# Optimization experiments

Hardware: AMD Instinct MI355X
Metric: run time of the kernel (lower is better)

The kernel has to match this reference:

```python
import jax, jax.numpy as jnp
import numpy as np

N_NODES = 100000


def gcn_conv(x, src, dst, W, b):
    # x: [N, F_in]; src/dst include self-loops; symmetric degree normalization (PyG GCNConv)
    n = x.shape[0]
    xw = x @ W  # [N, F_out]
    ones = jnp.ones(dst.shape[0], dtype=xw.dtype)
    deg = jax.ops.segment_sum(ones, dst, num_segments=n)  # in-degree incl. self-loop
    dinv = jnp.where(deg > 0, jax.lax.rsqrt(deg), 0.0)
    norm = dinv[src] * dinv[dst]  # [E]
    msg = xw[src] * norm[:, None]  # gather + per-edge scale
    out = jax.ops.segment_sum(msg, dst, num_segments=n)  # scatter-add aggregation
    return out + b


def setup_inputs() -> dict:
    key = jax.random.key(0)
    ks = jax.random.split(key, 6)
    F_in = 512
    E = 3200000
    x = jax.random.normal(ks[0], (N_NODES, F_in), dtype=jnp.float32)
    edge_index = jax.random.randint(ks[1], (2, E), 0, N_NODES, dtype=jnp.int64)
    W1 = jax.random.normal(ks[2], (F_in, 16), dtype=jnp.float32) * (1.0 / np.sqrt(F_in))
    b1 = jnp.zeros((16,), dtype=jnp.float32)
    W2 = jax.random.normal(ks[3], (16, 16), dtype=jnp.float32) * 0.25
    b2 = jnp.zeros((16,), dtype=jnp.float32)
    fc_w = jax.random.normal(ks[4], (16, 1), dtype=jnp.float32) * 0.25
    fc_b = jnp.zeros((1,), dtype=jnp.float32)
    return {"x": x, "edge_index": edge_index, "W1": W1, "b1": b1,
            "W2": W2, "b2": b2, "fc_w": fc_w, "fc_b": fc_b}


def reference(x, edge_index, W1, b1, W2, b2, fc_w, fc_b):
    n = x.shape[0]
    loop = jnp.arange(n, dtype=edge_index.dtype)
    src = jnp.concatenate([edge_index[0], loop])  # add self-loops
    dst = jnp.concatenate([edge_index[1], loop])
    h = jax.nn.relu(gcn_conv(x, src, dst, W1, b1))
    h = jax.nn.relu(gcn_conv(h, src, dst, W2, b2))
    g = jnp.mean(h, axis=0, keepdims=True)  # global_mean_pool, single graph -> [1, 16]
    return g @ fc_w + fc_b  # [1, 1]
```

## Files before the change

kernel.cpp:

```cpp
#include <hip/hip_runtime.h>
#include <hip/hip_fp16.h>
#include <stdint.h>

#define F_IN 512
#define F_OUT 16
#define CB_SHIFT 8
#define CB_W 256
#define PER 6250
#define SORT_CAP 6400

__device__ inline float4 f4_shfl_xor(float4 v, int mask) {
    float4 r;
    r.x = __shfl_xor(v.x, mask);
    r.y = __shfl_xor(v.y, mask);
    r.z = __shfl_xor(v.z, mask);
    r.w = __shfl_xor(v.w, mask);
    return r;
}

__device__ inline float4 ld_h4(const __half* __restrict__ xw, int s, int q) {
    const __half2* p = (const __half2*)(xw + ((size_t)s << 4)) + (q << 1);
    float2 f0 = __half22float2(p[0]);
    float2 f1 = __half22float2(p[1]);
    return make_float4(f0.x, f0.y, f1.x, f1.y);
}

__global__ __launch_bounds__(256) void k_chist(const int* __restrict__ ei, int E, int K1, int B,
                                               int* __restrict__ cntT) {
    __shared__ int h[512];
    int t = threadIdx.x;
    for (int i = t; i < K1; i += 256) h[i] = 0;
    __syncthreads();
    int e0 = blockIdx.x * PER, e1 = min(E, e0 + PER);
    for (int e = e0 + t; e < e1; e += 256)
        atomicAdd(&h[ei[(size_t)E + e] >> CB_SHIFT], 1);
    __syncthreads();
    for (int i = t; i < K1; i += 256) cntT[(size_t)i * B + blockIdx.x] = h[i];
}

__global__ __launch_bounds__(512) void k_btot(const int* __restrict__ cntT, int B, int K1,
                                              int* __restrict__ bucketBase, int* __restrict__ bucketCnt) {
    __shared__ int sm[512];
    int k = threadIdx.x;
    int tot = 0;
    if (k < K1) {
        const int4* row = (const int4*)(cntT + (size_t)k * B);
        for (int b = 0; b < B / 4; b++) {
            int4 v = row[b];
            tot += v.x + v.y + v.z + v.w;
        }
    }
    sm[k] = tot;
    __syncthreads();
    for (int off = 1; off < 512; off <<= 1) {
        int add = (k >= off) ? sm[k - off] : 0;
        __syncthreads();
        sm[k] += add;
        __syncthreads();
    }
    if (k < K1) { bucketBase[k] = sm[k] - tot; bucketCnt[k] = tot; }
}

__global__ __launch_bounds__(512) void k_bbase(const int* __restrict__ cntT, int B,
                                               const int* __restrict__ bucketBase,
                                               int* __restrict__ baseT) {
    __shared__ int sm[512];
    int k = blockIdx.x, t = threadIdx.x;
    int v = (t < B) ? cntT[(size_t)k * B + t] : 0;
    sm[t] = v;
    __syncthreads();
    for (int off = 1; off < 512; off <<= 1) {
        int add = (t >= off) ? sm[t - off] : 0;
        __syncthreads();
        sm[t] += add;
        __syncthreads();
    }
    if (t < B) baseT[(size_t)k * B + t] = bucketBase[k] + sm[t] - v;
}

__global__ __launch_bounds__(512) void k_csort(const int* __restrict__ ei, int E, int K1, int B,
                                               const int* __restrict__ baseT, unsigned* __restrict__ part) {
    __shared__ unsigned sorted[SORT_CAP];
    __shared__ int h[512], lb[512], cur[512], gb[512];
    int t = threadIdx.x;
    int e0 = blockIdx.x * PER, e1 = min(E, e0 + PER);
    h[t] = 0;
    __syncthreads();
    for (int e = e0 + t; e < e1; e += 512)
        atomicAdd(&h[ei[(size_t)E + e] >> CB_SHIFT], 1);
    __syncthreads();
    int v = h[t];
    lb[t] = v;
    __syncthreads();
    for (int off = 1; off < 512; off <<= 1) {
        int add = (t >= off) ? lb[t - off] : 0;
        __syncthreads();
        lb[t] += add;
        __syncthreads();
    }
    int excl = lb[t] - v;
    __syncthreads();
    lb[t] = excl;
    cur[t] = excl;
    if (t < K1) gb[t] = baseT[(size_t)t * B + blockIdx.x];
    __syncthreads();
    for (int e = e0 + t; e < e1; e += 512) {
        int s = ei[e];
        int d = ei[(size_t)E + e];
        int pos = atomicAdd(&cur[d >> CB_SHIFT], 1);
        sorted[pos] = ((unsigned)s << CB_SHIFT) | (unsigned)(d & (CB_W - 1));
    }
    __syncthreads();
    int g16 = t >> 4, ln = t & 15;
    for (int k = g16; k < K1; k += 32) {
        int s0 = lb[k];
        int s1 = cur[k];
        int g  = gb[k];
        for (int i = s0 + ln; i < s1; i += 16)
            part[(size_t)g + (i - s0)] = sorted[i];
    }
}

__global__ __launch_bounds__(512) void k_prep2(const unsigned* __restrict__ part,
                                               const int* __restrict__ bucketBase, const int* __restrict__ bucketCnt,
                                               int* __restrict__ hist, float* __restrict__ dinv,
                                               int* __restrict__ offsets, int* __restrict__ csr, int N) {
    __shared__ int fh[CB_W], fb[CB_W], cur[CB_W];
    int k = blockIdx.x, t = threadIdx.x;
    int base = bucketBase[k], cnt = bucketCnt[k];
    int d0 = k << CB_SHIFT;
    if (t < CB_W) fh[t] = 0;
    __syncthreads();
    for (int i = t; i < cnt; i += 512)
        atomicAdd(&fh[part[(size_t)base + i] & (CB_W - 1)], 1);
    __syncthreads();
    int v = 0;
    if (t < CB_W) { v = fh[t]; fb[t] = v; }
    __syncthreads();
    for (int off = 1; off < CB_W; off <<= 1) {
        int add = (t >= off && t < CB_W) ? fb[t - off] : 0;
        __syncthreads();
        if (t < CB_W) fb[t] += add;
        __syncthreads();
    }
    if (t < CB_W) {
        int excl = fb[t] - v;
        int n = d0 + t;
        if (n < N) {
            offsets[n] = base + excl;
            hist[n] = v;
            dinv[n] = rsqrtf((float)(v + 1));
        }
        cur[t] = excl;
    }
    __syncthreads();
    for (int i = t; i < cnt; i += 512) {
        unsigned e = part[(size_t)base + i];
        int pos = atomicAdd(&cur[e & (CB_W - 1)], 1);
        csr[(size_t)base + pos] = (int)(e >> CB_SHIFT);
    }
}

__global__ __launch_bounds__(256) void k_gemm1(const float* __restrict__ x, const float* __restrict__ W1,
                                               const float* __restrict__ dinv, __half* __restrict__ xw1p, int N) {
    int n = blockIdx.x * 256 + threadIdx.x;
    if (n >= N) return;
    const float4* xr = (const float4*)(x + (size_t)n * F_IN);
    const float4* wr = (const float4*)W1;

    float acc[16];
#pragma unroll
    for (int j = 0; j < 16; j++) acc[j] = 0.f;

#pragma unroll 4
    for (int kk = 0; kk < 128; kk++) {
        float4 xv = xr[kk];
#pragma unroll
        for (int i = 0; i < 4; i++) {
            float xs = (i == 0) ? xv.x : (i == 1) ? xv.y : (i == 2) ? xv.z : xv.w;
#pragma unroll
            for (int q = 0; q < 4; q++) {
                float4 wv = wr[kk * 16 + i * 4 + q];
                acc[q*4+0] = fmaf(xs, wv.x, acc[q*4+0]);
                acc[q*4+1] = fmaf(xs, wv.y, acc[q*4+1]);
                acc[q*4+2] = fmaf(xs, wv.z, acc[q*4+2]);
                acc[q*4+3] = fmaf(xs, wv.w, acc[q*4+3]);
            }
        }
    }
    float dn = dinv[n];
    __half2 o2[8];
#pragma unroll
    for (int j = 0; j < 8; j++)
        o2[j] = __floats2half2_rn(dn * acc[2*j], dn * acc[2*j + 1]);
    uint4* op = (uint4*)(xw1p + ((size_t)n << 4));
    op[0] = *(uint4*)&o2[0];
    op[1] = *(uint4*)&o2[4];
}

__global__ __launch_bounds__(256) void k_agg1(const __half* __restrict__ xw, const int* __restrict__ offsets,
                                              const int* __restrict__ hist, const float* __restrict__ dinv,
                                              const int* __restrict__ csr, const float* __restrict__ b1,
                                              const float* __restrict__ W2, __half* __restrict__ xw2p, int N) {
    __shared__ float W2s[256];
    if (threadIdx.x < 256) W2s[threadIdx.x] = W2[threadIdx.x];
    __syncthreads();

    int lane = threadIdx.x & 63;
    int wave = threadIdx.x >> 6;
    int grp  = lane >> 4;
    int sub  = lane & 15;
    int eo   = sub >> 2;
    int q    = sub & 3;
    int node = blockIdx.x * 16 + wave * 4 + grp;
    if (node >= N) return;

    int start = offsets[node], cnt = hist[node];
    float dn = dinv[node];
    float4 a0 = make_float4(0.f,0.f,0.f,0.f), a1 = a0, a2 = a0, a3 = a0;
    int i = 0;
    for (; i + 32 <= cnt; i += 32) {
        int s0 = csr[start + i + eo];
        int s1 = csr[start + i + 4 + eo];
        int s2 = csr[start + i + 8 + eo];
        int s3 = csr[start + i + 12 + eo];
        int s4 = csr[start + i + 16 + eo];
        int s5 = csr[start + i + 20 + eo];
        int s6 = csr[start + i + 24 + eo];
        int s7 = csr[start + i + 28 + eo];
        float4 v0 = ld_h4(xw, s0, q);
        float4 v1 = ld_h4(xw, s1, q);
        float4 v2 = ld_h4(xw, s2, q);
        float4 v3 = ld_h4(xw, s3, q);
        float4 v4 = ld_h4(xw, s4, q);
        float4 v5 = ld_h4(xw, s5, q);
        float4 v6 = ld_h4(xw, s6, q);
        float4 v7 = ld_h4(xw, s7, q);
        a0.x+=v0.x; a0.y+=v0.y; a0.z+=v0.z; a0.w+=v0.w;
        a1.x+=v1.x; a1.y+=v1.y; a1.z+=v1.z; a1.w+=v1.w;
        a2.x+=v2.x; a2.y+=v2.y; a2.z+=v2.z; a2.w+=v2.w;
        a3.x+=v3.x; a3.y+=v3.y; a3.z+=v3.z; a3.w+=v3.w;
        a0.x+=v4.x; a0.y+=v4.y; a0.z+=v4.z; a0.w+=v4.w;
        a1.x+=v5.x; a1.y+=v5.y; a1.z+=v5.z; a1.w+=v5.w;
        a2.x+=v6.x; a2.y+=v6.y; a2.z+=v6.z; a2.w+=v6.w;
        a3.x+=v7.x; a3.y+=v7.y; a3.z+=v7.z; a3.w+=v7.w;
    }
    for (; i + 16 <= cnt; i += 16) {
        int s0 = csr[start + i + eo];
        int s1 = csr[start + i + 4 + eo];
        int s2 = csr[start + i + 8 + eo];
        int s3 = csr[start + i + 12 + eo];
        float4 v0 = ld_h4(xw, s0, q);
        float4 v1 = ld_h4(xw, s1, q);
        float4 v2 = ld_h4(xw, s2, q);
        float4 v3 = ld_h4(xw, s3, q);
        a0.x+=v0.x; a0.y+=v0.y; a0.z+=v0.z; a0.w+=v0.w;
        a1.x+=v1.x; a1.y+=v1.y; a1.z+=v1.z; a1.w+=v1.w;
        a2.x+=v2.x; a2.y+=v2.y; a2.z+=v2.z; a2.w+=v2.w;
        a3.x+=v3.x; a3.y+=v3.y; a3.z+=v3.z; a3.w+=v3.w;
    }
    for (; i + 8 <= cnt; i += 8) {
        int s0 = csr[start + i + eo];
        int s1 = csr[start + i + 4 + eo];
        float4 v0 = ld_h4(xw, s0, q);
        float4 v1 = ld_h4(xw, s1, q);
        a0.x+=v0.x; a0.y+=v0.y; a0.z+=v0.z; a0.w+=v0.w;
        a1.x+=v1.x; a1.y+=v1.y; a1.z+=v1.z; a1.w+=v1.w;
    }
    for (; i < cnt; i += 4) {
        if (i + eo < cnt) {
            int s0 = csr[start + i + eo];
            float4 v0 = ld_h4(xw, s0, q);
            a0.x+=v0.x; a0.y+=v0.y; a0.z+=v0.z; a0.w+=v0.w;
        }
    }
    float4 acc;
    acc.x = a0.x+a1.x+a2.x+a3.x;
    acc.y = a0.y+a1.y+a2.y+a3.y;
    acc.z = a0.z+a1.z+a2.z+a3.z;
    acc.w = a0.w+a1.w+a2.w+a3.w;
    { float4 u = f4_shfl_xor(acc, 4); acc.x+=u.x; acc.y+=u.y; acc.z+=u.z; acc.w+=u.w; }
    { float4 u = f4_shfl_xor(acc, 8); acc.x+=u.x; acc.y+=u.y; acc.z+=u.z; acc.w+=u.w; }

    float4 sv = ld_h4(xw, node, q);
    float4 bq = ((const float4*)b1)[q];
    float4 h;
    h.x = fmaxf(dn * (acc.x + sv.x) + bq.x, 0.f);
    h.y = fmaxf(dn * (acc.y + sv.y) + bq.y, 0.f);
    h.z = fmaxf(dn * (acc.z + sv.z) + bq.z, 0.f);
    h.w = fmaxf(dn * (acc.w + sv.w) + bq.w, 0.f);

    float o = 0.f;
#pragma unroll
    for (int a = 0; a < 4; a++) {
        int src = (grp << 4) + a;
        float h0 = __shfl(h.x, src);
        float h1 = __shfl(h.y, src);
        float h2 = __shfl(h.z, src);
        float h3 = __shfl(h.w, src);
        o += h0 * W2s[(a*4+0)*16 + sub] + h1 * W2s[(a*4+1)*16 + sub]
           + h2 * W2s[(a*4+2)*16 + sub] + h3 * W2s[(a*4+3)*16 + sub];
    }
    xw2p[((size_t)node << 4) + sub] = __float2half_rn(dn * o);
}

__global__ __launch_bounds__(256) void k_agg2(const __half* __restrict__ xw, const int* __restrict__ offsets,
                                              const int* __restrict__ hist, const float* __restrict__ dinv,
                                              const int* __restrict__ csr, const float* __restrict__ b2,
                                              float* __restrict__ partials, int N) {
    int lane = threadIdx.x & 63;
    int wave = threadIdx.x >> 6;
    int grp  = lane >> 4;
    int sub  = lane & 15;
    int eo   = sub >> 2;
    int q    = sub & 3;
    int node = blockIdx.x * 16 + wave * 4 + grp;

    float4 m = make_float4(0.f, 0.f, 0.f, 0.f);
    if (node < N) {
        int start = offsets[node], cnt = hist[node];
        float dn = dinv[node];
        float4 a0 = make_float4(0.f,0.f,0.f,0.f), a1 = a0, a2 = a0, a3 = a0;
        int i = 0;
        for (; i + 32 <= cnt; i += 32) {
            int s0 = csr[start + i + eo];
            int s1 = csr[start + i + 4 + eo];
            int s2 = csr[start + i + 8 + eo];
            int s3 = csr[start + i + 12 + eo];
            int s4 = csr[start + i + 16 + eo];
            int s5 = csr[start + i + 20 + eo];
            int s6 = csr[start + i + 24 + eo];
            int s7 = csr[start + i + 28 + eo];
            float4 v0 = ld_h4(xw, s0, q);
            float4 v1 = ld_h4(xw, s1, q);
            float4 v2 = ld_h4(xw, s2, q);
            float4 v3 = ld_h4(xw, s3, q);
            float4 v4 = ld_h4(xw, s4, q);
            float4 v5 = ld_h4(xw, s5, q);
            float4 v6 = ld_h4(xw, s6, q);
            float4 v7 = ld_h4(xw, s7, q);
            a0.x+=v0.x; a0.y+=v0.y; a0.z+=v0.z; a0.w+=v0.w;
            a1.x+=v1.x; a1.y+=v1.y; a1.z+=v1.z; a1.w+=v1.w;
            a2.x+=v2.x; a2.y+=v2.y; a2.z+=v2.z; a2.w+=v2.w;
            a3.x+=v3.x; a3.y+=v3.y; a3.z+=v3.z; a3.w+=v3.w;
            a0.x+=v4.x; a0.y+=v4.y; a0.z+=v4.z; a0.w+=v4.w;
            a1.x+=v5.x; a1.y+=v5.y; a1.z+=v5.z; a1.w+=v5.w;
            a2.x+=v6.x; a2.y+=v6.y; a2.z+=v6.z; a2.w+=v6.w;
            a3.x+=v7.x; a3.y+=v7.y; a3.z+=v7.z; a3.w+=v7.w;
        }
        for (; i + 16 <= cnt; i += 16) {
            int s0 = csr[start + i + eo];
            int s1 = csr[start + i + 4 + eo];
            int s2 = csr[start + i + 8 + eo];
            int s3 = csr[start + i + 12 + eo];
            float4 v0 = ld_h4(xw, s0, q);
            float4 v1 = ld_h4(xw, s1, q);
            float4 v2 = ld_h4(xw, s2, q);
            float4 v3 = ld_h4(xw, s3, q);
            a0.x+=v0.x; a0.y+=v0.y; a0.z+=v0.z; a0.w+=v0.w;
            a1.x+=v1.x; a1.y+=v1.y; a1.z+=v1.z; a1.w+=v1.w;
            a2.x+=v2.x; a2.y+=v2.y; a2.z+=v2.z; a2.w+=v2.w;
            a3.x+=v3.x; a3.y+=v3.y; a3.z+=v3.z; a3.w+=v3.w;
        }
        for (; i + 8 <= cnt; i += 8) {
            int s0 = csr[start + i + eo];
            int s1 = csr[start + i + 4 + eo];
            float4 v0 = ld_h4(xw, s0, q);
            float4 v1 = ld_h4(xw, s1, q);
            a0.x+=v0.x; a0.y+=v0.y; a0.z+=v0.z; a0.w+=v0.w;
            a1.x+=v1.x; a1.y+=v1.y; a1.z+=v1.z; a1.w+=v1.w;
        }
        for (; i < cnt; i += 4) {
            if (i + eo < cnt) {
                int s0 = csr[start + i + eo];
                float4 v0 = ld_h4(xw, s0, q);
                a0.x+=v0.x; a0.y+=v0.y; a0.z+=v0.z; a0.w+=v0.w;
            }
        }
        float4 acc;
        acc.x = a0.x+a1.x+a2.x+a3.x;
        acc.y = a0.y+a1.y+a2.y+a3.y;
        acc.z = a0.z+a1.z+a2.z+a3.z;
        acc.w = a0.w+a1.w+a2.w+a3.w;
        { float4 u = f4_shfl_xor(acc, 4); acc.x+=u.x; acc.y+=u.y; acc.z+=u.z; acc.w+=u.w; }
        { float4 u = f4_shfl_xor(acc, 8); acc.x+=u.x; acc.y+=u.y; acc.z+=u.z; acc.w+=u.w; }
        float4 sv = ld_h4(xw, node, q);
        float4 bq = ((const float4*)b2)[q];
        if (eo == 0) {
            m.x = fmaxf(dn * (acc.x + sv.x) + bq.x, 0.f);
            m.y = fmaxf(dn * (acc.y + sv.y) + bq.y, 0.f);
            m.z = fmaxf(dn * (acc.z + sv.z) + bq.z, 0.f);
            m.w = fmaxf(dn * (acc.w + sv.w) + bq.w, 0.f);
        }
    }
    { float4 u = f4_shfl_xor(m, 16); m.x+=u.x; m.y+=u.y; m.z+=u.z; m.w+=u.w; }
    { float4 u = f4_shfl_xor(m, 32); m.x+=u.x; m.y+=u.y; m.z+=u.z; m.w+=u.w; }
    __shared__ float smf[4][16];
    if (lane < 4) {
        smf[wave][q*4+0] = m.x;
        smf[wave][q*4+1] = m.y;
        smf[wave][q*4+2] = m.z;
        smf[wave][q*4+3] = m.w;
    }
    __syncthreads();
    if (threadIdx.x < 16) {
        float s = smf[0][threadIdx.x] + smf[1][threadIdx.x] + smf[2][threadIdx.x] + smf[3][threadIdx.x];
        partials[(size_t)blockIdx.x * 16 + threadIdx.x] = s;
    }
}

__global__ void k_final(const float* __restrict__ partials, int NB, const float* __restrict__ fc_w,
                        const float* __restrict__ fc_b, float* __restrict__ out, float invN) {
    __shared__ float sm[64][16];
    int t = threadIdx.x;
    int g = t >> 4, j = t & 15;
    float s = 0.0f;
    for (int bk = g; bk < NB; bk += 64) s += partials[(size_t)bk * 16 + j];
    sm[g][j] = s;
    __syncthreads();
    for (int str = 32; str > 0; str >>= 1) {
        if (g < str) sm[g][j] += sm[g + str][j];
        __syncthreads();
    }
    if (t == 0) {
        float acc = fc_b[0];
#pragma unroll
        for (int jj = 0; jj < 16; jj++) acc += sm[0][jj] * invN * fc_w[jj];
        out[0] = acc;
    }
}

extern "C" void kernel_launch(void* const* d_in, const int* in_sizes, int n_in,
                              void* d_out, int out_size, void* d_ws, size_t ws_size,
                              hipStream_t stream) {
    const float* x   = (const float*)d_in[0];
    const int*   ei  = (const int*)d_in[1];
    const float* W1  = (const float*)d_in[2];
    const float* b1  = (const float*)d_in[3];
    const float* W2  = (const float*)d_in[4];
    const float* b2  = (const float*)d_in[5];
    const float* fcw = (const float*)d_in[6];
    const float* fcb = (const float*)d_in[7];
    float* out = (float*)d_out;

    int N = in_sizes[0] / F_IN;
    int E = in_sizes[1] / 2;
    int K1 = (N + CB_W - 1) >> CB_SHIFT;
    int B1 = (E + PER - 1) / PER;

    char* p = (char*)d_ws;
    auto alloc = [&](size_t bytes) {
        void* r = (void*)p;
        p += (bytes + 255) & ~(size_t)255;
        return r;
    };
    int*   cntT       = (int*)alloc((size_t)K1 * B1 * 4);
    int*   baseT      = (int*)alloc((size_t)K1 * B1 * 4);
    int*   bucketBase = (int*)alloc((size_t)K1 * 4);
    int*   bucketCnt  = (int*)alloc((size_t)K1 * 4);
    int*   hist       = (int*)alloc((size_t)N * 4);
    int*   offsets    = (int*)alloc((size_t)N * 4);
    float* dinv       = (float*)alloc((size_t)N * 4);
    int*   csr        = (int*)alloc((size_t)E * 4);
    unsigned* part    = (unsigned*)alloc((size_t)E * 4);
    __half* xw1p      = (__half*)alloc((size_t)N * F_OUT * 2);
    __half* xw2p      = (__half*)alloc((size_t)N * F_OUT * 2);
    int NB_NODE = (N + 15) / 16;
    float* partials = (float*)alloc((size_t)NB_NODE * 16 * 4);

    k_chist<<<B1, 256, 0, stream>>>(ei, E, K1, B1, cntT);
    k_btot<<<1, 512, 0, stream>>>(cntT, B1, K1, bucketBase, bucketCnt);
    k_bbase<<<K1, 512, 0, stream>>>(cntT, B1, bucketBase, baseT);
    k_csort<<<B1, 512, 0, stream>>>(ei, E, K1, B1, baseT, part);
    k_prep2<<<K1, 512, 0, stream>>>(part, bucketBase, bucketCnt, hist, dinv, offsets, csr, N);

    k_gemm1<<<(N + 255) / 256, 256, 0, stream>>>(x, W1, dinv, xw1p, N);
    k_agg1<<<NB_NODE, 256, 0, stream>>>(xw1p, offsets, hist, dinv, csr, b1, W2, xw2p, N);
    k_agg2<<<NB_NODE, 256, 0, stream>>>(xw2p, offsets, hist, dinv, csr, b2, partials, N);
    k_final<<<1, 1024, 0, stream>>>(partials, NB_NODE, fcw, fcb, out, 1.0f / (float)N);
}
```

Before: 218.5 us.

## Merge CSR finalize and X@W1 GEMM into one launch, defer dinv scaling

The CSR finalization (prep2) and the first-layer GEMM now share one kernel launch, split by block index, so the independent GEMM blocks can run alongside the per-bucket degree/CSR work. The dinv dependency is removed from the GEMM: it writes unscaled fp16 xw1, and a new small k_scale kernel multiplies by dinv afterwards. This adds an extra read and write of xw1 (and an extra fp16 rounding step), and uses 512-thread blocks for the GEMM instead of 256.

```diff
diff --git a/kernel.cpp b/kernel.cpp
--- a/kernel.cpp
+++ b/kernel.cpp
@@ -121,81 +121,97 @@
     }
 }
 
-__global__ __launch_bounds__(512) void k_prep2(const unsigned* __restrict__ part,
+__global__ __launch_bounds__(512) void k_prepg(const unsigned* __restrict__ part,
                                                const int* __restrict__ bucketBase, const int* __restrict__ bucketCnt,
                                                int* __restrict__ hist, float* __restrict__ dinv,
-                                               int* __restrict__ offsets, int* __restrict__ csr, int N) {
-    __shared__ int fh[CB_W], fb[CB_W], cur[CB_W];
-    int k = blockIdx.x, t = threadIdx.x;
-    int base = bucketBase[k], cnt = bucketCnt[k];
-    int d0 = k << CB_SHIFT;
-    if (t < CB_W) fh[t] = 0;
-    __syncthreads();
-    for (int i = t; i < cnt; i += 512)
-        atomicAdd(&fh[part[(size_t)base + i] & (CB_W - 1)], 1);
-    __syncthreads();
-    int v = 0;
-    if (t < CB_W) { v = fh[t]; fb[t] = v; }
-    __syncthreads();
-    for (int off = 1; off < CB_W; off <<= 1) {
-        int add = (t >= off && t < CB_W) ? fb[t - off] : 0;
-        __syncthreads();
-        if (t < CB_W) fb[t] += add;
-        __syncthreads();
-    }
-    if (t < CB_W) {
-        int excl = fb[t] - v;
-        int n = d0 + t;
-        if (n < N) {
-            offsets[n] = base + excl;
-            hist[n] = v;
-            dinv[n] = rsqrtf((float)(v + 1));
-        }
-        cur[t] = excl;
-    }
-    __syncthreads();
-    for (int i = t; i < cnt; i += 512) {
-        unsigned e = part[(size_t)base + i];
-        int pos = atomicAdd(&cur[e & (CB_W - 1)], 1);
-        csr[(size_t)base + pos] = (int)(e >> CB_SHIFT);
-    }
-}
-
-__global__ __launch_bounds__(256) void k_gemm1(const float* __restrict__ x, const float* __restrict__ W1,
-                                               const float* __restrict__ dinv, __half* __restrict__ xw1p, int N) {
-    int n = blockIdx.x * 256 + threadIdx.x;
-    if (n >= N) return;
-    const float4* xr = (const float4*)(x + (size_t)n * F_IN);
-    const float4* wr = (const float4*)W1;
-
-    float acc[16];
-#pragma unroll
-    for (int j = 0; j < 16; j++) acc[j] = 0.f;
+                                               int* __restrict__ offsets, int* __restrict__ csr,
+                                               const float* __restrict__ x, const float* __restrict__ W1,
+                                               __half* __restrict__ xw1p, int N, int K1) {
+    if ((int)blockIdx.x < K1) {
+        __shared__ int fh[CB_W], fb[CB_W], cur[CB_W];
+        int k = blockIdx.x, t = threadIdx.x;
+        int base = bucketBase[k], cnt = bucketCnt[k];
+        int d0 = k << CB_SHIFT;
+        if (t < CB_W) fh[t] = 0;
+        __syncthreads();
+        for (int i = t; i < cnt; i += 512)
+            atomicAdd(&fh[part[(size_t)base + i] & (CB_W - 1)], 1);
+        __syncthreads();
+        int v = 0;
+        if (t < CB_W) { v = fh[t]; fb[t] = v; }
+        __syncthreads();
+        for (int off = 1; off < CB_W; off <<= 1) {
+            int add = (t >= off && t < CB_W) ? fb[t - off] : 0;
+            __syncthreads();
+            if (t < CB_W) fb[t] += add;
+            __syncthreads();
+        }
+        if (t < CB_W) {
+            int excl = fb[t] - v;
+            int n = d0 + t;
+            if (n < N) {
+                offsets[n] = base + excl;
+                hist[n] = v;
+                dinv[n] = rsqrtf((float)(v + 1));
+            }
+            cur[t] = excl;
+        }
+        __syncthreads();
+        for (int i = t; i < cnt; i += 512) {
+            unsigned e = part[(size_t)base + i];
+            int pos = atomicAdd(&cur[e & (CB_W - 1)], 1);
+            csr[(size_t)base + pos] = (int)(e >> CB_SHIFT);
+        }
+    } else {
+        int n = ((int)blockIdx.x - K1) * 512 + (int)threadIdx.x;
+        if (n >= N) return;
+        const float4* xr = (const float4*)(x + (size_t)n * F_IN);
+        const float4* wr = (const float4*)W1;
+
+        float acc[16];
+#pragma unroll
+        for (int j = 0; j < 16; j++) acc[j] = 0.f;
 
 #pragma unroll 4
-    for (int kk = 0; kk < 128; kk++) {
-        float4 xv = xr[kk];
-#pragma unroll
-        for (int i = 0; i < 4; i++) {
-            float xs = (i == 0) ? xv.x : (i == 1) ? xv.y : (i == 2) ? xv.z : xv.w;
-#pragma unroll
-            for (int q = 0; q < 4; q++) {
-                float4 wv = wr[kk * 16 + i * 4 + q];
-                acc[q*4+0] = fmaf(xs, wv.x, acc[q*4+0]);
-                acc[q*4+1] = fmaf(xs, wv.y, acc[q*4+1]);
-                acc[q*4+2] = fmaf(xs, wv.z, acc[q*4+2]);
-                acc[q*4+3] = fmaf(xs, wv.w, acc[q*4+3]);
+        for (int kk = 0; kk < 128; kk++) {
+            float4 xv = xr[kk];
+#pragma unroll
+            for (int i = 0; i < 4; i++) {
+                float xs = (i == 0) ? xv.x : (i == 1) ? xv.y : (i == 2) ? xv.z : xv.w;
+#pragma unroll
+                for (int q = 0; q < 4; q++) {
+                    float4 wv = wr[kk * 16 + i * 4 + q];
+                    acc[q*4+0] = fmaf(xs, wv.x, acc[q*4+0]);
+                    acc[q*4+1] = fmaf(xs, wv.y, acc[q*4+1]);
+                    acc[q*4+2] = fmaf(xs, wv.z, acc[q*4+2]);
+                    acc[q*4+3] = fmaf(xs, wv.w, acc[q*4+3]);
+                }
             }
         }
-    }
-    float dn = dinv[n];
-    __half2 o2[8];
-#pragma unroll
-    for (int j = 0; j < 8; j++)
-        o2[j] = __floats2half2_rn(dn * acc[2*j], dn * acc[2*j + 1]);
-    uint4* op = (uint4*)(xw1p + ((size_t)n << 4));
-    op[0] = *(uint4*)&o2[0];
-    op[1] = *(uint4*)&o2[4];
+        __half2 o2[8];
+#pragma unroll
+        for (int j = 0; j < 8; j++)
+            o2[j] = __floats2half2_rn(acc[2*j], acc[2*j + 1]);
+        uint4* op = (uint4*)(xw1p + ((size_t)n << 4));
+        op[0] = *(uint4*)&o2[0];
+        op[1] = *(uint4*)&o2[4];
+    }
+}
+
+__global__ __launch_bounds__(512) void k_scale(__half* __restrict__ xw, const float* __restrict__ dinv, int N) {
+    int i = blockIdx.x * 512 + threadIdx.x;
+    if (i < N * 2) {
+        float dn = dinv[i >> 1];
+        uint4* p = (uint4*)xw + i;
+        uint4 v = *p;
+        __half2* h = (__half2*)&v;
+#pragma unroll
+        for (int j = 0; j < 4; j++) {
+            float2 f = __half22float2(h[j]);
+            h[j] = __floats2half2_rn(f.x * dn, f.y * dn);
+        }
+        *p = v;
+    }
 }
 
 __global__ __launch_bounds__(256) void k_agg1(const __half* __restrict__ xw, const int* __restrict__ offsets,
@@ -468,13 +484,16 @@
     int NB_NODE = (N + 15) / 16;
     float* partials = (float*)alloc((size_t)NB_NODE * 16 * 4);
 
+    int GB = (N + 511) / 512;
+
     k_chist<<<B1, 256, 0, stream>>>(ei, E, K1, B1, cntT);
     k_btot<<<1, 512, 0, stream>>>(cntT, B1, K1, bucketBase, bucketCnt);
     k_bbase<<<K1, 512, 0, stream>>>(cntT, B1, bucketBase, baseT);
     k_csort<<<B1, 512, 0, stream>>>(ei, E, K1, B1, baseT, part);
-    k_prep2<<<K1, 512, 0, stream>>>(part, bucketBase, bucketCnt, hist, dinv, offsets, csr, N);
-
-    k_gemm1<<<(N + 255) / 256, 256, 0, stream>>>(x, W1, dinv, xw1p, N);
+    k_prepg<<<K1 + GB, 512, 0, stream>>>(part, bucketBase, bucketCnt, hist, dinv, offsets, csr,
+                                         x, W1, xw1p, N, K1);
+    k_scale<<<(2 * N + 511) / 512, 512, 0, stream>>>(xw1p, dinv, N);
+
     k_agg1<<<NB_NODE, 256, 0, stream>>>(xw1p, offsets, hist, dinv, csr, b1, W2, xw2p, N);
     k_agg2<<<NB_NODE, 256, 0, stream>>>(xw2p, offsets, hist, dinv, csr, b2, partials, N);
     k_final<<<1, 1024, 0, stream>>>(partials, NB_NODE, fcw, fcb, out, 1.0f / (float)N);
```

Result: no change. 220.2 us (+0.8%).

## Stage x tiles through shared memory in gemm1 for coalesced loads

Applied to the files above, without the earlier changes.

The first GEMM previously had each thread read its own 2KB row of x, so adjacent threads hit addresses 2KB apart and loads were uncoalesced. It now loads 32-column chunks of 240 rows cooperatively into padded shared memory with coalesced float4 loads, and stages the matching W1 slice in shared memory. The cost is two block barriers per chunk, 16 idle threads per block, and float4 reads from a 33-stride padded tile that may be misaligned or conflict.

```diff
diff --git a/kernel.cpp b/kernel.cpp
--- a/kernel.cpp
+++ b/kernel.cpp
@@ -8,6 +8,7 @@
 #define CB_W 256
 #define PER 6250
 #define SORT_CAP 6400
+#define TROWS 240
 
 __device__ inline float4 f4_shfl_xor(float4 v, int mask) {
     float4 r;
@@ -163,39 +164,68 @@
 
 __global__ __launch_bounds__(256) void k_gemm1(const float* __restrict__ x, const float* __restrict__ W1,
                                                const float* __restrict__ dinv, __half* __restrict__ xw1p, int N) {
-    int n = blockIdx.x * 256 + threadIdx.x;
-    if (n >= N) return;
-    const float4* xr = (const float4*)(x + (size_t)n * F_IN);
-    const float4* wr = (const float4*)W1;
+    __shared__ float  xt[TROWS * 33];
+    __shared__ float4 Wc[128];
+
+    int t = threadIdx.x;
+    int rowBase = blockIdx.x * TROWS;
+    int myRow = rowBase + t;
+    bool active = (t < TROWS) && (myRow < N);
 
     float acc[16];
 #pragma unroll
     for (int j = 0; j < 16; j++) acc[j] = 0.f;
 
-#pragma unroll 4
-    for (int kk = 0; kk < 128; kk++) {
-        float4 xv = xr[kk];
-#pragma unroll
-        for (int i = 0; i < 4; i++) {
-            float xs = (i == 0) ? xv.x : (i == 1) ? xv.y : (i == 2) ? xv.z : xv.w;
-#pragma unroll
-            for (int q = 0; q < 4; q++) {
-                float4 wv = wr[kk * 16 + i * 4 + q];
-                acc[q*4+0] = fmaf(xs, wv.x, acc[q*4+0]);
-                acc[q*4+1] = fmaf(xs, wv.y, acc[q*4+1]);
-                acc[q*4+2] = fmaf(xs, wv.z, acc[q*4+2]);
-                acc[q*4+3] = fmaf(xs, wv.w, acc[q*4+3]);
+    const float4* w1v = (const float4*)W1;
+
+    for (int c = 0; c < 16; c++) {
+        __syncthreads();
+#pragma unroll
+        for (int s = 0; s < 8; s++) {
+            int idx = (s << 8) + t;
+            if (idx < TROWS * 8) {
+                int r = idx >> 3, c4 = idx & 7;
+                int gr = rowBase + r;
+                float4 v = make_float4(0.f, 0.f, 0.f, 0.f);
+                if (gr < N) v = ((const float4*)(x + (size_t)gr * F_IN + c * 32))[c4];
+                *(float4*)&xt[r * 33 + c4 * 4] = v;
             }
         }
-    }
-    float dn = dinv[n];
-    __half2 o2[8];
-#pragma unroll
-    for (int j = 0; j < 8; j++)
-        o2[j] = __floats2half2_rn(dn * acc[2*j], dn * acc[2*j + 1]);
-    uint4* op = (uint4*)(xw1p + ((size_t)n << 4));
-    op[0] = *(uint4*)&o2[0];
-    op[1] = *(uint4*)&o2[4];
+        if (t < 128) Wc[t] = w1v[c * 128 + t];
+        __syncthreads();
+
+        if (active) {
+            const float* xr = &xt[t * 33];
+#pragma unroll
+            for (int kk = 0; kk < 8; kk++) {
+                float4 xv = *(const float4*)&xr[kk * 4];
+                const float4* wr = &Wc[(kk * 4) * 4];
+#pragma unroll
+                for (int i = 0; i < 4; i++) {
+                    float xs = (i == 0) ? xv.x : (i == 1) ? xv.y : (i == 2) ? xv.z : xv.w;
+#pragma unroll
+                    for (int q = 0; q < 4; q++) {
+                        float4 wv = wr[i * 4 + q];
+                        acc[q*4+0] = fmaf(xs, wv.x, acc[q*4+0]);
+                        acc[q*4+1] = fmaf(xs, wv.y, acc[q*4+1]);
+                        acc[q*4+2] = fmaf(xs, wv.z, acc[q*4+2]);
+                        acc[q*4+3] = fmaf(xs, wv.w, acc[q*4+3]);
+                    }
+                }
+            }
+        }
+    }
+
+    if (active) {
+        float dn = dinv[myRow];
+        __half2 o2[8];
+#pragma unroll
+        for (int j = 0; j < 8; j++)
+            o2[j] = __floats2half2_rn(dn * acc[2*j], dn * acc[2*j + 1]);
+        uint4* op = (uint4*)(xw1p + ((size_t)myRow << 4));
+        op[0] = *(uint4*)&o2[0];
+        op[1] = *(uint4*)&o2[4];
+    }
 }
 
 __global__ __launch_bounds__(256) void k_agg1(const __half* __restrict__ xw, const int* __restrict__ offsets,
@@ -474,7 +504,7 @@
     k_csort<<<B1, 512, 0, stream>>>(ei, E, K1, B1, baseT, part);
     k_prep2<<<K1, 512, 0, stream>>>(part, bucketBase, bucketCnt, hist, dinv, offsets, csr, N);
 
-    k_gemm1<<<(N + 255) / 256, 256, 0, stream>>>(x, W1, dinv, xw1p, N);
+    k_gemm1<<<(N + TROWS - 1) / TROWS, 256, 0, stream>>>(x, W1, dinv, xw1p, N);
     k_agg1<<<NB_NODE, 256, 0, stream>>>(xw1p, offsets, hist, dinv, csr, b1, W2, xw2p, N);
     k_agg2<<<NB_NODE, 256, 0, stream>>>(xw2p, offsets, hist, dinv, csr, b2, partials, N);
     k_final<<<1, 1024, 0, stream>>>(partials, NB_NODE, fcw, fcb, out, 1.0f / (float)N);
```

Result: slower. 299.4 us (+37.0%).

## Compute first-layer GEMM with bf16 MFMA per wavefront over 16-row tiles

Applied to the files above, without the earlier changes.

Replaces the one-thread-per-row scalar FMA GEMM for x@W1 with a wave-per-16-row-tile kernel using the 16x16x32 bf16 MFMA instruction. W1 is converted to bf16 fragments held in registers, and x rows are converted on the fly. A fixed persistent grid loops over tiles. The old access pattern had each thread read its own 2 KB row, which coalesces poorly; the new one has lanes read adjacent 32-byte chunks. It trades fp32 precision for bf16 inputs, and the output stores become scattered 2-byte writes.

```diff
diff --git a/kernel.cpp b/kernel.cpp
--- a/kernel.cpp
+++ b/kernel.cpp
@@ -8,6 +8,9 @@
 #define CB_W 256
 #define PER 6250
 #define SORT_CAP 6400
+
+typedef __attribute__((ext_vector_type(8))) short bf16x8;
+typedef __attribute__((ext_vector_type(4))) float f32x4;
 
 __device__ inline float4 f4_shfl_xor(float4 v, int mask) {
     float4 r;
@@ -16,6 +19,12 @@
     r.z = __shfl_xor(v.z, mask);
     r.w = __shfl_xor(v.w, mask);
     return r;
+}
+
+__device__ inline short f2bf(float f) {
+    unsigned u = __float_as_uint(f);
+    unsigned r = (u + 0x7FFFu + ((u >> 16) & 1u)) >> 16;
+    return (short)(unsigned short)r;
 }
 
 __device__ inline float4 ld_h4(const __half* __restrict__ xw, int s, int q) {
@@ -161,41 +170,47 @@
     }
 }
 
-__global__ __launch_bounds__(256) void k_gemm1(const float* __restrict__ x, const float* __restrict__ W1,
-                                               const float* __restrict__ dinv, __half* __restrict__ xw1p, int N) {
-    int n = blockIdx.x * 256 + threadIdx.x;
-    if (n >= N) return;
-    const float4* xr = (const float4*)(x + (size_t)n * F_IN);
-    const float4* wr = (const float4*)W1;
-
-    float acc[16];
-#pragma unroll
-    for (int j = 0; j < 16; j++) acc[j] = 0.f;
-
-#pragma unroll 4
-    for (int kk = 0; kk < 128; kk++) {
-        float4 xv = xr[kk];
-#pragma unroll
-        for (int i = 0; i < 4; i++) {
-            float xs = (i == 0) ? xv.x : (i == 1) ? xv.y : (i == 2) ? xv.z : xv.w;
-#pragma unroll
-            for (int q = 0; q < 4; q++) {
-                float4 wv = wr[kk * 16 + i * 4 + q];
-                acc[q*4+0] = fmaf(xs, wv.x, acc[q*4+0]);
-                acc[q*4+1] = fmaf(xs, wv.y, acc[q*4+1]);
-                acc[q*4+2] = fmaf(xs, wv.z, acc[q*4+2]);
-                acc[q*4+3] = fmaf(xs, wv.w, acc[q*4+3]);
+__global__ __launch_bounds__(256, 4) void k_gemm1(const float* __restrict__ x, const float* __restrict__ W1,
+                                                  const float* __restrict__ dinv, __half* __restrict__ xw1p, int N) {
+    int lane = threadIdx.x & 63;
+    int wv   = blockIdx.x * 4 + (threadIdx.x >> 6);
+    int nw   = gridDim.x * 4;
+    int r16  = lane & 15;
+    int kg   = lane >> 4;
+
+    bf16x8 bfrag[16];
+#pragma unroll
+    for (int s = 0; s < 16; s++) {
+        bf16x8 f;
+#pragma unroll
+        for (int i = 0; i < 8; i++)
+            f[i] = f2bf(W1[(s * 32 + kg * 8 + i) * 16 + r16]);
+        bfrag[s] = f;
+    }
+
+    int ntiles = (N + 15) >> 4;
+    for (int tile = wv; tile < ntiles; tile += nw) {
+        int rowA = (tile << 4) + r16;
+        const float* xr = x + (size_t)min(rowA, N - 1) * F_IN + kg * 8;
+        f32x4 acc = {0.f, 0.f, 0.f, 0.f};
+#pragma unroll
+        for (int s = 0; s < 16; s++) {
+            float4 xa = *(const float4*)(xr + s * 32);
+            float4 xb = *(const float4*)(xr + s * 32 + 4);
+            bf16x8 af;
+            af[0] = f2bf(xa.x); af[1] = f2bf(xa.y); af[2] = f2bf(xa.z); af[3] = f2bf(xa.w);
+            af[4] = f2bf(xb.x); af[5] = f2bf(xb.y); af[6] = f2bf(xb.z); af[7] = f2bf(xb.w);
+            acc = __builtin_amdgcn_mfma_f32_16x16x32_bf16(af, bfrag[s], acc, 0, 0, 0);
+        }
+#pragma unroll
+        for (int j = 0; j < 4; j++) {
+            int row = (tile << 4) + kg * 4 + j;
+            if (row < N) {
+                float dn = dinv[row];
+                xw1p[((size_t)row << 4) + r16] = __float2half_rn(dn * acc[j]);
             }
         }
     }
-    float dn = dinv[n];
-    __half2 o2[8];
-#pragma unroll
-    for (int j = 0; j < 8; j++)
-        o2[j] = __floats2half2_rn(dn * acc[2*j], dn * acc[2*j + 1]);
-    uint4* op = (uint4*)(xw1p + ((size_t)n << 4));
-    op[0] = *(uint4*)&o2[0];
-    op[1] = *(uint4*)&o2[4];
 }
 
 __global__ __launch_bounds__(256) void k_agg1(const __half* __restrict__ xw, const int* __restrict__ offsets,
@@ -474,7 +489,7 @@
     k_csort<<<B1, 512, 0, stream>>>(ei, E, K1, B1, baseT, part);
     k_prep2<<<K1, 512, 0, stream>>>(part, bucketBase, bucketCnt, hist, dinv, offsets, csr, N);
 
-    k_gemm1<<<(N + 255) / 256, 256, 0, stream>>>(x, W1, dinv, xw1p, N);
+    k_gemm1<<<782, 256, 0, stream>>>(x, W1, dinv, xw1p, N);
     k_agg1<<<NB_NODE, 256, 0, stream>>>(xw1p, offsets, hist, dinv, csr, b1, W2, xw2p, N);
     k_agg2<<<NB_NODE, 256, 0, stream>>>(xw2p, offsets, hist, dinv, csr, b2, partials, N);
     k_final<<<1, 1024, 0, stream>>>(partials, NB_NODE, fcw, fcb, out, 1.0f / (float)N);
```

Result: no change. 214.5 us (-1.8%).
